# Performance work log

Measured on AMD Instinct MI355X. Metric: run time of the kernel, lower is better.

The kernel has to match this reference:

```python
import jax, jax.numpy as jnp
import numpy as np

STRIDE = (1, 1)
PAD = (1, 1)


def setup_inputs() -> dict:
    key = jax.random.key(0)
    k1, k2, k3 = jax.random.split(key, 3)
    X = jax.random.normal(k1, (32, 32, 224, 224), dtype=jnp.float32)
    W = jax.random.normal(k2, (32, 32, 3, 3), dtype=jnp.float32)
    b = jax.random.normal(k3, (32,), dtype=jnp.float32)
    return {"X": X, "W": W, "b": b}


def reference(X, W, b):
    # Equivalent of the module's im2col + GEMM conv (A @ [W_flat.T; b]):
    # a standard NCHW conv2d with bias, stride=1, padding=1, dilation=1, groups=1.
    Y = jax.lax.conv_general_dilated(
        X, W,
        window_strides=STRIDE,
        padding=[(PAD[0], PAD[0]), (PAD[1], PAD[1])],
        dimension_numbers=("NCHW", "OIHW", "NCHW"),
    )
    return Y + b[None, :, None, None]
```

## Files before the change

### kernel.cpp

```cpp
#include <hip/hip_runtime.h>

typedef __attribute__((ext_vector_type(4))) float float4v;
typedef __attribute__((ext_vector_type(4))) float f32x4;
typedef __attribute__((ext_vector_type(8))) short short8;
typedef __attribute__((ext_vector_type(16))) float f32x16;

#define C_IN 32
#define C_OUT 32
#define HH 224
#define WW 224
#define HW (HH * WW)
#define STRIPE 28
#define RING_PX 226
#define PIX_STRIDE 80
#define ROW_BYTES (RING_PX * PIX_STRIDE)
#define NTHR 512

__device__ __forceinline__ short f2bf(float f) {
    unsigned u = __float_as_uint(f);
    u += 0x7FFFu + ((u >> 16) & 1u);
    return (short)(u >> 16);
}
__device__ __forceinline__ unsigned pack2(float e, float o) {
    return (unsigned)(unsigned short)f2bf(e) | ((unsigned)(unsigned short)f2bf(o) << 16);
}

#define BAR() do {                                             \
        asm volatile("s_waitcnt lgkmcnt(0)" ::: "memory");     \
        __builtin_amdgcn_s_barrier();                          \
    } while (0)

__global__ __launch_bounds__(NTHR) __attribute__((amdgpu_waves_per_eu(4, 4)))
void conv3x3_rows(const float* __restrict__ X, const float* __restrict__ Wt,
                  const float* __restrict__ Bias, float* __restrict__ Y) {
    __shared__ __align__(16) char ring0[ROW_BYTES];
    __shared__ __align__(16) char ring1[ROW_BYTES];
    __shared__ __align__(16) char ring2[ROW_BYTES];
    __shared__ __align__(16) char wlds[18 * 1024];
    __shared__ __align__(16) float blds[32];
    __shared__ __align__(16) float ybuf[C_OUT * WW];

    const int tid = threadIdx.x;
    const int lane = tid & 63;
    const int wid = tid >> 6;
    const int col = lane & 31;
    const int khalf = lane >> 5;

    if (tid < 64) {
#pragma unroll
        for (int rs = 0; rs < 9; ++rs) {
#pragma unroll
            for (int ch = 0; ch < 2; ++ch) {
                short8 f;
#pragma unroll
                for (int j = 0; j < 8; ++j) {
                    int c = ch * 16 + (tid >> 5) * 8 + j;
                    f[j] = f2bf(Wt[((tid & 31) * C_IN + c) * 9 + rs]);
                }
                *(short8*)(wlds + (rs * 2 + ch) * 1024 + tid * 16) = f;
            }
        }
    }
    if (tid < 32) {
        int kh = tid >> 4, i = tid & 15;
        blds[tid] = Bias[(i & 3) + 8 * (i >> 2) + 4 * kh];
    }

    const int cp0 = tid & 15, w40 = tid >> 4;
    const int t1 = tid + NTHR;
    const bool has1 = (tid < 896 - NTHR);
    const int cp1 = t1 & 15, w41 = t1 >> 4;
    const int ge0 = (2 * cp0) * HW + 4 * w40;
    const int go0 = ge0 + HW;
    const int ge1 = (2 * cp1) * HW + 4 * w41;
    const int go1 = ge1 + HW;

    const int bid = blockIdx.x;
    const int n = bid >> 3;
    const int h1 = (bid & 7) * STRIPE;
    const float* Xn = X + n * C_IN * HW;

    const short8 z8 = {0, 0, 0, 0, 0, 0, 0, 0};

#define STAGE_ROW(hh, sb) do {                                     \
        const float* rp = Xn + (hh) * WW;                          \
        float4v e0 = *(const float4v*)(rp + ge0);                  \
        float4v o0 = *(const float4v*)(rp + go0);                  \
        float4v e1, o1;                                            \
        if (has1) {                                                \
            e1 = *(const float4v*)(rp + ge1);                      \
            o1 = *(const float4v*)(rp + go1);                      \
        }                                                          \
        char* wb0 = (sb) + (1 + 4 * w40) * PIX_STRIDE + cp0 * 4;   \
        *(unsigned*)(wb0                  ) = pack2(e0[0], o0[0]); \
        *(unsigned*)(wb0 +     PIX_STRIDE ) = pack2(e0[1], o0[1]); \
        *(unsigned*)(wb0 + 2 * PIX_STRIDE ) = pack2(e0[2], o0[2]); \
        *(unsigned*)(wb0 + 3 * PIX_STRIDE ) = pack2(e0[3], o0[3]); \
        if (has1) {                                                \
            char* wb1 = (sb) + (1 + 4 * w41) * PIX_STRIDE + cp1 * 4; \
            *(unsigned*)(wb1                  ) = pack2(e1[0], o1[0]); \
            *(unsigned*)(wb1 +     PIX_STRIDE ) = pack2(e1[1], o1[1]); \
            *(unsigned*)(wb1 + 2 * PIX_STRIDE ) = pack2(e1[2], o1[2]); \
            *(unsigned*)(wb1 + 3 * PIX_STRIDE ) = pack2(e1[3], o1[3]); \
        }                                                          \
        if (tid < 8) {   \
            int px = (tid < 4) ? 0 : (RING_PX - 1);                \
            *(short8*)((sb) + px * PIX_STRIDE + (tid & 3) * 16) = z8; \
        }                                                          \
    } while (0)

#define ZERO_ROW(sb) do {                                          \
        for (int i = tid; i < ROW_BYTES / 16; i += NTHR)           \
            *(short8*)((sb) + i * 16) = z8;                        \
    } while (0)

#pragma unroll
    for (int j = 0; j < 3; ++j) {
        int hh = h1 - 1 + j;
        char* sb = (j == 0) ? ring0 : (j == 1) ? ring1 : ring2;
        if (hh >= 0) {
            STAGE_ROW(hh, sb);
        } else {
            ZERO_ROW(sb);
        }
    }
    __syncthreads();

    char *rA = ring0, *rB = ring1, *rC = ring2;
    const int pcol = col * PIX_STRIDE + khalf * 16;

    for (int h = h1; h < h1 + STRIPE; ++h) {
        const int hh = h + 2;
        const bool do_pref = (hh <= h1 + STRIPE);
        const bool validrow = do_pref && (hh < HH);

        if (wid < 7) {
            const int px0 = wid * 32;
            f32x16 acc;
#pragma unroll
            for (int j = 0; j < 4; ++j) {
                f32x4 bb = *(const f32x4*)(blds + khalf * 16 + j * 4);
#pragma unroll
                for (int k = 0; k < 4; ++k) acc[j * 4 + k] = bb[k];
            }
            const int pb = px0 * PIX_STRIDE + pcol;
#pragma unroll
            for (int rs = 0; rs < 9; ++rs) {
                const int r = rs / 3, s = rs - 3 * r;
                const char* rb = (r == 0) ? rA : (r == 1) ? rB : rC;
                const int addr = pb + s * PIX_STRIDE;
#pragma unroll
                for (int ch = 0; ch < 2; ++ch) {
                    short8 wf = *(const short8*)(wlds + (rs * 2 + ch) * 1024 + lane * 16);
                    short8 bf = *(const short8*)(rb + addr + ch * 32);
                    acc = __builtin_amdgcn_mfma_f32_32x32x16_bf16(wf, bf, acc, 0, 0, 0);
                }
            }
            const int px = px0 + col;
#pragma unroll
            for (int i = 0; i < 16; ++i) {
                int ko = (i & 3) + 8 * (i >> 2) + 4 * khalf;
                ybuf[ko * WW + px] = acc[i];
            }
        }

        BAR();

        {
            float* Yr = Y + n * C_OUT * HW + h * WW;
#pragma unroll
            for (int it = 0; it < 4; ++it) {
                int u = tid + it * NTHR;
                if (u < C_OUT * 56) {
                    f32x4 v = *(const f32x4*)(ybuf + u * 4);
                    int ko = u / 56, rem = u - ko * 56;
                    __builtin_nontemporal_store(v, (float4v*)(Yr + ko * HW + rem * 4));
                }
            }
        }

        if (validrow) {
            STAGE_ROW(hh, rA);
        } else if (do_pref) {
            ZERO_ROW(rA);
        }

        BAR();

        char* t = rA; rA = rB; rB = rC; rC = t;
    }
#undef STAGE_ROW
#undef ZERO_ROW
}

extern "C" void kernel_launch(void* const* d_in, const int* in_sizes, int n_in,
                              void* d_out, int out_size, void* d_ws, size_t ws_size,
                              hipStream_t stream) {
    const float* X = (const float*)d_in[0];
    const float* W = (const float*)d_in[1];
    const float* B = (const float*)d_in[2];
    float* Y = (float*)d_out;
    conv3x3_rows<<<dim3(256), dim3(NTHR), 0, stream>>>(X, W, B, Y);
}
```

Measured before the change: 78.91 us.

## Use a four-row input ring and double-buffered output to halve barriers

The three-row ring becomes a four-row ring indexed by row modulo four, and the output staging buffer is double-buffered. Each iteration now stores the previous row's output, computes the current row and prefetches the next input row, all under a single barrier. The goal is to remove one barrier per row and let global stores and loads overlap with the MFMA work. The cost is much more LDS per block (about 148 KB), which keeps the kernel at one block per CU, plus an extra flush after the loop.

```diff
diff --git a/kernel.cpp b/kernel.cpp
--- a/kernel.cpp
+++ b/kernel.cpp
@@ -33,12 +33,11 @@
 __global__ __launch_bounds__(NTHR) __attribute__((amdgpu_waves_per_eu(4, 4)))
 void conv3x3_rows(const float* __restrict__ X, const float* __restrict__ Wt,
                   const float* __restrict__ Bias, float* __restrict__ Y) {
-    __shared__ __align__(16) char ring0[ROW_BYTES];
-    __shared__ __align__(16) char ring1[ROW_BYTES];
-    __shared__ __align__(16) char ring2[ROW_BYTES];
+    __shared__ __align__(16) char ring[4 * ROW_BYTES];
     __shared__ __align__(16) char wlds[18 * 1024];
     __shared__ __align__(16) float blds[32];
-    __shared__ __align__(16) float ybuf[C_OUT * WW];
+    __shared__ __align__(16) float ybuf0[C_OUT * WW];
+    __shared__ __align__(16) float ybuf1[C_OUT * WW];
 
     const int tid = threadIdx.x;
     const int lane = tid & 63;
@@ -79,6 +78,7 @@
     const int n = bid >> 3;
     const int h1 = (bid & 7) * STRIPE;
     const float* Xn = X + n * C_IN * HW;
+    float* Yn = Y + n * C_OUT * HW;
 
     const short8 z8 = {0, 0, 0, 0, 0, 0, 0, 0};
 
@@ -114,10 +114,23 @@
             *(short8*)((sb) + i * 16) = z8;                        \
     } while (0)
 
+#define FLUSH_ROW(hf, yb) do {                                     \
+        float* Yr = Yn + (hf) * WW;                                \
+        _Pragma("unroll")                                          \
+        for (int it = 0; it < 4; ++it) {                           \
+            int u = tid + it * NTHR;                               \
+            if (u < C_OUT * 56) {                                  \
+                f32x4 v = *(const f32x4*)((yb) + u * 4);           \
+                int ko = u / 56, rem = u - ko * 56;                \
+                __builtin_nontemporal_store(v, (float4v*)(Yr + ko * HW + rem * 4)); \
+            }                                                      \
+        }                                                          \
+    } while (0)
+
 #pragma unroll
     for (int j = 0; j < 3; ++j) {
         int hh = h1 - 1 + j;
-        char* sb = (j == 0) ? ring0 : (j == 1) ? ring1 : ring2;
+        char* sb = ring + (hh & 3) * ROW_BYTES;
         if (hh >= 0) {
             STAGE_ROW(hh, sb);
         } else {
@@ -126,7 +139,6 @@
     }
     __syncthreads();
 
-    char *rA = ring0, *rB = ring1, *rC = ring2;
     const int pcol = col * PIX_STRIDE + khalf * 16;
 
     for (int h = h1; h < h1 + STRIPE; ++h) {
@@ -134,6 +146,11 @@
         const bool do_pref = (hh <= h1 + STRIPE);
         const bool validrow = do_pref && (hh < HH);
 
+        if (h > h1) {
+            const float* yb = ((h - 1) & 1) ? ybuf1 : ybuf0;
+            FLUSH_ROW(h - 1, yb);
+        }
+
         if (wid < 7) {
             const int px0 = wid * 32;
             f32x16 acc;
@@ -143,11 +160,14 @@
 #pragma unroll
                 for (int k = 0; k < 4; ++k) acc[j * 4 + k] = bb[k];
             }
+            const char* r0p = ring + ((h - 1) & 3) * ROW_BYTES;
+            const char* r1p = ring + ((h    ) & 3) * ROW_BYTES;
+            const char* r2p = ring + ((h + 1) & 3) * ROW_BYTES;
             const int pb = px0 * PIX_STRIDE + pcol;
 #pragma unroll
             for (int rs = 0; rs < 9; ++rs) {
                 const int r = rs / 3, s = rs - 3 * r;
-                const char* rb = (r == 0) ? rA : (r == 1) ? rB : rC;
+                const char* rb = (r == 0) ? r0p : (r == 1) ? r1p : r2p;
                 const int addr = pb + s * PIX_STRIDE;
 #pragma unroll
                 for (int ch = 0; ch < 2; ++ch) {
@@ -156,41 +176,32 @@
                     acc = __builtin_amdgcn_mfma_f32_32x32x16_bf16(wf, bf, acc, 0, 0, 0);
                 }
             }
+            float* yb = (h & 1) ? ybuf1 : ybuf0;
             const int px = px0 + col;
 #pragma unroll
             for (int i = 0; i < 16; ++i) {
                 int ko = (i & 3) + 8 * (i >> 2) + 4 * khalf;
-                ybuf[ko * WW + px] = acc[i];
-            }
+                yb[ko * WW + px] = acc[i];
+            }
+        }
+
+        if (validrow) {
+            STAGE_ROW(hh, ring + (hh & 3) * ROW_BYTES);
+        } else if (do_pref) {
+            ZERO_ROW(ring + (hh & 3) * ROW_BYTES);
         }
 
         BAR();
-
-        {
-            float* Yr = Y + n * C_OUT * HW + h * WW;
-#pragma unroll
-            for (int it = 0; it < 4; ++it) {
-                int u = tid + it * NTHR;
-                if (u < C_OUT * 56) {
-                    f32x4 v = *(const f32x4*)(ybuf + u * 4);
-                    int ko = u / 56, rem = u - ko * 56;
-                    __builtin_nontemporal_store(v, (float4v*)(Yr + ko * HW + rem * 4));
-                }
-            }
-        }
-
-        if (validrow) {
-            STAGE_ROW(hh, rA);
-        } else if (do_pref) {
-            ZERO_ROW(rA);
-        }
-
-        BAR();
-
-        char* t = rA; rA = rB; rB = rC; rC = t;
+    }
+
+    {
+        const int hl = h1 + STRIPE - 1;
+        const float* yb = (hl & 1) ? ybuf1 : ybuf0;
+        FLUSH_ROW(hl, yb);
     }
 #undef STAGE_ROW
 #undef ZERO_ROW
+#undef FLUSH_ROW
 }
 
 extern "C" void kernel_launch(void* const* d_in, const int* in_sizes, int n_in,
```

Measured after the change: 78.89 us, median of 2. Within noise of the previous version (-0.0%).
